# Optimization experiments

Hardware: AMD Instinct MI355X
Metric: run time of the kernel (lower is better)

## Reference

```python
import jax, jax.numpy as jnp
import numpy as np

B, T, D = 4, 2048, 1024
H, DK = 8, 64
EPS = 1e-6

def _xavier(key, shape):
    fan_in, fan_out = shape[1], shape[0]
    lim = float(np.sqrt(6.0 / (fan_in + fan_out)))
    return jax.random.uniform(key, shape, jnp.float32, -lim, lim)

def setup_inputs() -> dict:
    key = jax.random.key(0)
    ks = jax.random.split(key, 7)
    x = jax.random.normal(ks[0], (B, T, D), jnp.float32)
    W_Q = _xavier(ks[1], (H * DK, D))
    W_K = _xavier(ks[2], (H * DK, D))
    W_V = _xavier(ks[3], (H * DK, D))
    W_g_w = _xavier(ks[4], (H * DK, D))
    W_g_b = jax.random.normal(ks[5], (H * DK,), jnp.float32) * 0.02
    W_O = _xavier(ks[6], (D, H * DK))
    decay_log = jnp.zeros((H,), jnp.float32)
    return {"x": x, "W_Q": W_Q, "W_K": W_K, "W_V": W_V,
            "W_g_w": W_g_w, "W_g_b": W_g_b, "W_O": W_O,
            "decay_log": decay_log}

def _phi(u):
    # ELU + 1 feature map (positive)
    return jax.nn.elu(u) + 1.0

def reference(x, W_Q, W_K, W_V, W_g_w, W_g_b, W_O, decay_log):
    b, t, d = x.shape
    q = _phi((x @ W_Q.T).reshape(b, t, H, DK))
    k = _phi((x @ W_K.T).reshape(b, t, H, DK))
    v = (x @ W_V.T).reshape(b, t, H, DK)
    gamma = jax.nn.sigmoid(decay_log)           # [H]
    g4 = gamma[None, :, None, None]             # [1,H,1,1]
    g3 = gamma[None, :, None]                   # [1,H,1]

    # time-major for scan: [T,B,H,DK]
    qT = jnp.moveaxis(q, 1, 0)
    kT = jnp.moveaxis(k, 1, 0)
    vT = jnp.moveaxis(v, 1, 0)

    S0 = jnp.zeros((b, H, DK, DK), x.dtype)
    z0 = jnp.zeros((b, H, DK), x.dtype)

    def step(carry, inp):
        S, z = carry
        qt, kt, vt = inp
        S = g4 * S + jnp.einsum('bhi,bhj->bhij', kt, vt)
        z = g3 * z + kt
        num = jnp.einsum('bhij,bhi->bhj', S, qt)
        den = jnp.sum(z * qt, axis=-1, keepdims=True) + EPS
        return (S, z), num / den

    _, ys = jax.lax.scan(step, (S0, z0), (qT, kT, vT))  # ys: [T,B,H,DK]
    outputs = jnp.moveaxis(ys, 0, 1)                    # [B,T,H,DK]

    gate = jax.nn.sigmoid(x @ W_g_w.T + W_g_b).reshape(b, t, H, DK)
    y = (outputs * gate).reshape(b, t, H * DK)
    return y @ W_O.T
```

## Files before the change

kernel.cpp:

```cpp
#include <hip/hip_runtime.h>
#include <cstdint>
#include <cstddef>

#define B_   4
#define T_   2048
#define D_   1024
#define H_   8
#define DK_  64
#define HD_  512
#define CH_  64
#define NC_  32
#define EPS_ 1e-6f

typedef __attribute__((ext_vector_type(4))) float f32x4;
typedef __attribute__((ext_vector_type(8))) short s16x8;

__device__ __forceinline__ unsigned short f2bf(float f) {
    unsigned int x = __float_as_uint(f);
    unsigned int r = (x + 0x7FFFu + ((x >> 16) & 1u)) >> 16;
    return (unsigned short)r;
}
__device__ __forceinline__ float bf2f(unsigned short u) {
    return __uint_as_float(((unsigned int)u) << 16);
}
__device__ __forceinline__ void ld4(const float* p, float* o) {
    float4 v = *(const float4*)p; o[0]=v.x; o[1]=v.y; o[2]=v.z; o[3]=v.w;
}
__device__ __forceinline__ void gl_lds16(const unsigned short* g, unsigned short* l) {
    __builtin_amdgcn_global_load_lds(
        (const __attribute__((address_space(1))) unsigned int*)g,
        (__attribute__((address_space(3))) unsigned int*)l, 16, 0, 0);
}

__global__ __launch_bounds__(256) void k_cvt_all(
    const float* __restrict__ x,
    const float* __restrict__ wq, const float* __restrict__ wk,
    const float* __restrict__ wv, const float* __restrict__ wgw,
    const float* __restrict__ wo,
    unsigned short* __restrict__ xb,
    unsigned short* __restrict__ wqb, unsigned short* __restrict__ wkb,
    unsigned short* __restrict__ wvb, unsigned short* __restrict__ wgb,
    unsigned short* __restrict__ wob)
{
    int bid = blockIdx.x;
    const float* src; unsigned short* dst; int idx;
    if (bid < 8192) {
        src = x; dst = xb; idx = bid * 256 + threadIdx.x;
    } else {
        int r = bid - 8192;
        int w = r >> 9;
        idx = (r & 511) * 256 + threadIdx.x;
        switch (w) {
            case 0:  src = wq;  dst = wqb; break;
            case 1:  src = wk;  dst = wkb; break;
            case 2:  src = wv;  dst = wvb; break;
            case 3:  src = wgw; dst = wgb; break;
            default: src = wo;  dst = wob; break;
        }
    }
    float4 v = ((const float4*)src)[idx];
    ushort4 o;
    o.x = f2bf(v.x); o.y = f2bf(v.y); o.z = f2bf(v.z); o.w = f2bf(v.w);
    ((ushort4*)dst)[idx] = o;
}


__global__ __launch_bounds__(512, 2) void k_gemm_qkvg(
    const unsigned short* __restrict__ xb,
    const unsigned short* __restrict__ wqb, const unsigned short* __restrict__ wkb,
    const unsigned short* __restrict__ wvb, const unsigned short* __restrict__ wgb,
    const float* __restrict__ bias,
    unsigned short* __restrict__ qo, unsigned short* __restrict__ ko,
    unsigned short* __restrict__ vo, unsigned short* __restrict__ go)
{
    __shared__ unsigned short As[2][256 * 64];
    __shared__ unsigned short Bs[2][256 * 64];
    const int tid = threadIdx.x;
    const int id  = blockIdx.x;
    const int xcd = id & 7, per = id >> 3;
    const int mtile = xcd * 4 + (per & 3);
    const int ntile = per >> 2;
    const int which = ntile >> 1;
    const int nb    = ntile & 1;
    const int m0    = mtile * 256;
    const int n0    = nb * 256;
    const unsigned short* Wp = (which == 0) ? wqb : (which == 1) ? wkb : (which == 2) ? wvb : wgb;
    unsigned short* Op       = (which == 0) ? qo  : (which == 1) ? ko  : (which == 2) ? vo  : go;
    const int K = D_;
    const int NIT = K / 64;

    const int lane = tid & 63, wave = tid >> 6;
    const int wm = (wave >> 2) * 128, wn = (wave & 3) * 64;
    const int r16 = lane & 15, quad = lane >> 4;
    const int lrow = lane >> 3, lseg = lane & 7;
    const int sseg = lseg ^ lrow;
    const int rx   = r16 & 7;

    f32x4 acc[8][4];
    #pragma unroll
    for (int a = 0; a < 8; a++)
        #pragma unroll
        for (int b = 0; b < 4; b++) acc[a][b] = 0.0f;

    auto stage = [&](int buf, int ko_) {
        #pragma unroll
        for (int i = 0; i < 4; i++) {
            int chunk = wave * 4 + i;
            int row = chunk * 8 + lrow;
            gl_lds16(xb + (size_t)(m0 + row) * K + ko_ + sseg * 8, &As[buf][chunk * 512]);
            gl_lds16(Wp + (size_t)(n0 + row) * K + ko_ + sseg * 8, &Bs[buf][chunk * 512]);
        }
    };

    stage(0, 0);
    for (int it = 0; it < NIT; ++it) {
        if (it + 1 < NIT) {
            stage((it + 1) & 1, (it + 1) * 64);
            asm volatile("s_waitcnt vmcnt(8)" ::: "memory");
        } else {
            asm volatile("s_waitcnt vmcnt(0)" ::: "memory");
        }
        __builtin_amdgcn_s_barrier();
        const int buf = it & 1;
        #pragma unroll
        for (int kk = 0; kk < 64; kk += 32) {
            const int gb_ = kk >> 3;
            s16x8 af[8], bf[4];
            #pragma unroll
            for (int mt = 0; mt < 8; mt++)
                af[mt] = *(const s16x8*)&As[buf][(wm + mt * 16 + r16) * 64 + (((gb_ + quad) ^ rx) << 3)];
            #pragma unroll
            for (int nt = 0; nt < 4; nt++)
                bf[nt] = *(const s16x8*)&Bs[buf][(wn + nt * 16 + r16) * 64 + (((gb_ + quad) ^ rx) << 3)];
            #pragma unroll
            for (int mt = 0; mt < 8; mt++)
                #pragma unroll
                for (int nt = 0; nt < 4; nt++)
                    acc[mt][nt] = __builtin_amdgcn_mfma_f32_16x16x32_bf16(af[mt], bf[nt], acc[mt][nt], 0, 0, 0);
        }
        __builtin_amdgcn_s_barrier();
    }
    #pragma unroll
    for (int mt = 0; mt < 8; mt++) {
        #pragma unroll
        for (int nt = 0; nt < 4; nt++) {
            int col = n0 + wn + nt * 16 + r16;
            float bv = (which == 3) ? bias[col] : 0.0f;
            #pragma unroll
            for (int r = 0; r < 4; r++) {
                int row = m0 + wm + mt * 16 + quad * 4 + r;
                float v = acc[mt][nt][r];
                if (which <= 1)      v = (v > 0.0f) ? v + 1.0f : __builtin_expf(v);
                else if (which == 3) v = 1.0f / (1.0f + __builtin_expf(-(v + bv)));
                Op[(size_t)row * HD_ + col] = f2bf(v);
            }
        }
    }
}

__global__ __launch_bounds__(512, 2) void k_gemm_out(
    const unsigned short* __restrict__ ogb, const unsigned short* __restrict__ wob,
    float* __restrict__ y)
{
    __shared__ unsigned short As[2][256 * 64];
    __shared__ unsigned short Bs[2][128 * 64];
    const int tid = threadIdx.x;
    const int id  = blockIdx.x;
    const int xcd = id & 7, per = id >> 3;
    const int m0 = (xcd * 4 + (per & 3)) * 256;
    const int n0 = (per >> 2) * 128;
    const int K = HD_;
    const int NIT = K / 64;

    const int lane = tid & 63, wave = tid >> 6;
    const int wm = (wave >> 1) * 64, wn = (wave & 1) * 64;
    const int r16 = lane & 15, quad = lane >> 4;
    const int lrow = lane >> 3, lseg = lane & 7;
    const int sseg = lseg ^ lrow;
    const int rx   = r16 & 7;

    f32x4 acc[4][4];
    #pragma unroll
    for (int a = 0; a < 4; a++)
        #pragma unroll
        for (int b = 0; b < 4; b++) acc[a][b] = 0.0f;

    auto stage = [&](int buf, int ko_) {
        #pragma unroll
        for (int i = 0; i < 4; i++) {
            int chunk = wave * 4 + i;
            int row = chunk * 8 + lrow;
            gl_lds16(ogb + (size_t)(m0 + row) * K + ko_ + sseg * 8, &As[buf][chunk * 512]);
        }
        #pragma unroll
        for (int i = 0; i < 2; i++) {
            int chunk = wave * 2 + i;
            int row = chunk * 8 + lrow;
            gl_lds16(wob + (size_t)(n0 + row) * K + ko_ + sseg * 8, &Bs[buf][chunk * 512]);
        }
    };

    stage(0, 0);
    for (int it = 0; it < NIT; ++it) {
        if (it + 1 < NIT) {
            stage((it + 1) & 1, (it + 1) * 64);
            asm volatile("s_waitcnt vmcnt(6)" ::: "memory");
        } else {
            asm volatile("s_waitcnt vmcnt(0)" ::: "memory");
        }
        __builtin_amdgcn_s_barrier();
        const int buf = it & 1;
        #pragma unroll
        for (int kk = 0; kk < 64; kk += 32) {
            const int gb_ = kk >> 3;
            s16x8 af[4], bf[4];
            #pragma unroll
            for (int mt = 0; mt < 4; mt++)
                af[mt] = *(const s16x8*)&As[buf][(wm + mt * 16 + r16) * 64 + (((gb_ + quad) ^ rx) << 3)];
            #pragma unroll
            for (int nt = 0; nt < 4; nt++)
                bf[nt] = *(const s16x8*)&Bs[buf][(wn + nt * 16 + r16) * 64 + (((gb_ + quad) ^ rx) << 3)];
            #pragma unroll
            for (int mt = 0; mt < 4; mt++)
                #pragma unroll
                for (int nt = 0; nt < 4; nt++)
                    acc[mt][nt] = __builtin_amdgcn_mfma_f32_16x16x32_bf16(af[mt], bf[nt], acc[mt][nt], 0, 0, 0);
        }
        __builtin_amdgcn_s_barrier();
    }
    #pragma unroll
    for (int mt = 0; mt < 4; mt++)
        #pragma unroll
        for (int nt = 0; nt < 4; nt++) {
            int col = n0 + wn + nt * 16 + r16;
            #pragma unroll
            for (int r = 0; r < 4; r++) {
                int row = m0 + wm + mt * 16 + quad * 4 + r;
                y[(size_t)row * D_ + col] = acc[mt][nt][r];
            }
        }
}

__global__ __launch_bounds__(256) void k_chunk_sums(
    const unsigned short* __restrict__ Kb, const unsigned short* __restrict__ Vb,
    float* __restrict__ Ssum, float* __restrict__ zsum, const float* __restrict__ decay_log)
{
    __shared__ float kl[CH_ * 68];
    __shared__ float vl[CH_ * 68];
    const int tid = threadIdx.x;
    const int bc  = blockIdx.x;
    const int c   = bc & (NC_ - 1);
    const int bh  = bc >> 5;
    const int h   = bh & (H_ - 1);
    const int b   = bh >> 3;
    const float g  = 1.0f / (1.0f + __builtin_expf(-decay_log[h]));
    const float lg = __builtin_log2f(g);
    const int t0 = c * CH_;

    #pragma unroll
    for (int e = 0; e < 2; e++) {
        int lid = e * 256 + tid;
        int l = lid >> 3, d0 = (lid & 7) * 8;
        float w = __builtin_exp2f((float)(CH_ - 1 - l) * lg);
        size_t gidx = (size_t)(b * T_ + t0 + l) * HD_ + h * DK_ + d0;
        uint4 kraw = *(const uint4*)(Kb + gidx);
        uint4 vraw = *(const uint4*)(Vb + gidx);
        const unsigned short* kp = (const unsigned short*)&kraw;
        const unsigned short* vp = (const unsigned short*)&vraw;
        #pragma unroll
        for (int j = 0; j < 8; j++) {
            kl[l * 68 + d0 + j] = bf2f(kp[j]) * w;
            vl[l * 68 + d0 + j] = bf2f(vp[j]);
        }
    }
    __syncthreads();

    const int ti = tid >> 4, tj = tid & 15;
    const int i0 = ti * 4, j0 = tj * 4;
    float acc[4][4];
    #pragma unroll
    for (int r = 0; r < 4; r++)
        #pragma unroll
        for (int cc = 0; cc < 4; cc++) acc[r][cc] = 0.0f;

    for (int l = 0; l < CH_; l++) {
        float kv[4], vv[4];
        ld4(&kl[l * 68 + i0], kv);
        ld4(&vl[l * 68 + j0], vv);
        #pragma unroll
        for (int r = 0; r < 4; r++)
            #pragma unroll
            for (int cc = 0; cc < 4; cc++) acc[r][cc] += kv[r] * vv[cc];
    }
    size_t base = (size_t)bc * (DK_ * DK_);
    #pragma unroll
    for (int r = 0; r < 4; r++) {
        float4 st = make_float4(acc[r][0], acc[r][1], acc[r][2], acc[r][3]);
        *(float4*)&Ssum[base + (size_t)(i0 + r) * DK_ + j0] = st;
    }
    if (tid < DK_) {
        float s = 0.0f;
        for (int l = 0; l < CH_; l++) s += kl[l * 68 + tid];
        zsum[(size_t)bc * DK_ + tid] = s;
    }
}

__global__ __launch_bounds__(128) void k_chunk_scan(
    float* __restrict__ Ssum, float* __restrict__ zsum, const float* __restrict__ decay_log)
{
    const int tid = threadIdx.x;
    const int grp = blockIdx.x & 31;
    const int bh  = blockIdx.x >> 5;
    const int h   = bh & (H_ - 1);
    const float g  = 1.0f / (1.0f + __builtin_expf(-decay_log[h]));
    const float gC = __builtin_exp2f((float)CH_ * __builtin_log2f(g));
    int elem = grp * 128 + tid;
    float s = 0.0f;
    for (int c = 0; c < NC_; c++) {
        size_t idx = ((size_t)(bh * NC_ + c)) * 4096 + elem;
        float v = Ssum[idx];
        Ssum[idx] = s;
        s = gC * s + v;
    }
    if (grp == 0 && tid < DK_) {
        float z = 0.0f;
        for (int c = 0; c < NC_; c++) {
            size_t idx = ((size_t)(bh * NC_ + c)) * DK_ + tid;
            float v = zsum[idx];
            zsum[idx] = z;
            z = gC * z + v;
        }
    }
}

__global__ __launch_bounds__(256) void k_chunk_out(
    const unsigned short* __restrict__ Qb, const unsigned short* __restrict__ Kb,
    const unsigned short* __restrict__ Vb, const unsigned short* __restrict__ Gb,
    const float* __restrict__ Ssum, const float* __restrict__ zsum,
    unsigned short* __restrict__ OGb, const float* __restrict__ decay_log)
{
    __shared__ float BufA[CH_ * 68];
    __shared__ float BufB[CH_ * 68];
    __shared__ float BufC[CH_ * 68];
    __shared__ float den_l[CH_];
    __shared__ float zp_l[DK_];
    __shared__ float gpow[CH_ + 1];

    const int tid = threadIdx.x;
    const int bc  = blockIdx.x;
    const int c   = bc & (NC_ - 1);
    const int bh  = bc >> 5;
    const int h   = bh & (H_ - 1);
    const int b   = bh >> 3;
    const float g  = 1.0f / (1.0f + __builtin_expf(-decay_log[h]));
    const float lg = __builtin_log2f(g);
    const int t0 = c * CH_;

    if (tid <= CH_) gpow[tid] = __builtin_exp2f((float)tid * lg);
    if (tid < DK_)  zp_l[tid] = zsum[(size_t)bc * DK_ + tid];

    #pragma unroll
    for (int e = 0; e < 2; e++) {
        int lid = e * 256 + tid;
        int l = lid >> 3, d0 = (lid & 7) * 8;
        size_t gidx = (size_t)(b * T_ + t0 + l) * HD_ + h * DK_ + d0;
        uint4 qraw = *(const uint4*)(Qb + gidx);
        uint4 kraw = *(const uint4*)(Kb + gidx);
        const unsigned short* qp = (const unsigned short*)&qraw;
        const unsigned short* kp = (const unsigned short*)&kraw;
        #pragma unroll
        for (int j = 0; j < 8; j++) {
            BufA[(d0 + j) * 68 + l] = bf2f(qp[j]);
            BufB[(d0 + j) * 68 + l] = bf2f(kp[j]);
        }
    }
    {
        size_t base = (size_t)bc * 4096;
        #pragma unroll
        for (int e = 0; e < 4; e++) {
            int flat = (e * 256 + tid) * 4;
            int row = flat >> 6, c0 = flat & 63;
            *(float4*)&BufC[row * 68 + c0] = *(const float4*)&Ssum[base + flat];
        }
    }
    __syncthreads();

    const int ti = tid >> 4, tj = tid & 15;
    const int i0 = ti * 4, j0 = tj * 4;
    float sc[4][4], it[4][4];
    #pragma unroll
    for (int r = 0; r < 4; r++)
        #pragma unroll
        for (int cc = 0; cc < 4; cc++) { sc[r][cc] = 0.0f; it[r][cc] = 0.0f; }

    for (int d = 0; d < DK_; d++) {
        float qv[4], kv[4], sv[4];
        ld4(&BufA[d * 68 + i0], qv);
        ld4(&BufB[d * 68 + j0], kv);
        ld4(&BufC[d * 68 + j0], sv);
        #pragma unroll
        for (int r = 0; r < 4; r++)
            #pragma unroll
            for (int cc = 0; cc < 4; cc++) {
                sc[r][cc] += qv[r] * kv[cc];
                it[r][cc] += qv[r] * sv[cc];
            }
    }
    #pragma unroll
    for (int r = 0; r < 4; r++) {
        int i = i0 + r;
        #pragma unroll
        for (int cc = 0; cc < 4; cc++) {
            int jl = j0 + cc;
            sc[r][cc] = (jl <= i) ? sc[r][cc] * gpow[i - jl] : 0.0f;
            it[r][cc] *= gpow[i + 1];
        }
        float rs = sc[r][0] + sc[r][1] + sc[r][2] + sc[r][3];
        rs += __shfl_xor(rs, 1);
        rs += __shfl_xor(rs, 2);
        rs += __shfl_xor(rs, 4);
        rs += __shfl_xor(rs, 8);
        if (tj == 0) den_l[i] = rs;
    }
    __syncthreads();
    if (tid < DK_) {
        float dp = 0.0f;
        for (int d = 0; d < DK_; d++) dp += BufA[d * 68 + tid] * zp_l[d];
        den_l[tid] += gpow[tid + 1] * dp + EPS_;
    }
    __syncthreads();
    #pragma unroll
    for (int cc = 0; cc < 4; cc++) {
        float4 st = make_float4(sc[0][cc], sc[1][cc], sc[2][cc], sc[3][cc]);
        *(float4*)&BufA[(j0 + cc) * 68 + i0] = st;
    }
    #pragma unroll
    for (int e = 0; e < 2; e++) {
        int lid = e * 256 + tid;
        int l = lid >> 3, d0 = (lid & 7) * 8;
        size_t gidx = (size_t)(b * T_ + t0 + l) * HD_ + h * DK_ + d0;
        uint4 vraw = *(const uint4*)(Vb + gidx);
        const unsigned short* vp = (const unsigned short*)&vraw;
        #pragma unroll
        for (int j = 0; j < 8; j++) BufB[l * 68 + d0 + j] = bf2f(vp[j]);
    }
    __syncthreads();

    float og[4][4];
    #pragma unroll
    for (int r = 0; r < 4; r++)
        #pragma unroll
        for (int cc = 0; cc < 4; cc++) og[r][cc] = it[r][cc];

    for (int jl = 0; jl < CH_; jl++) {
        float scv[4], vv[4];
        ld4(&BufA[jl * 68 + i0], scv);
        ld4(&BufB[jl * 68 + j0], vv);
        #pragma unroll
        for (int r = 0; r < 4; r++)
            #pragma unroll
            for (int cc = 0; cc < 4; cc++) og[r][cc] += scv[r] * vv[cc];
    }
    #pragma unroll
    for (int r = 0; r < 4; r++) {
        int i = i0 + r;
        float rcp = 1.0f / den_l[i];
        size_t gidx = (size_t)(b * T_ + t0 + i) * HD_ + h * DK_ + j0;
        ushort4 graw = *(const ushort4*)(Gb + gidx);
        ushort4 o;
        o.x = f2bf(og[r][0] * rcp * bf2f(graw.x));
        o.y = f2bf(og[r][1] * rcp * bf2f(graw.y));
        o.z = f2bf(og[r][2] * rcp * bf2f(graw.z));
        o.w = f2bf(og[r][3] * rcp * bf2f(graw.w));
        *(ushort4*)(OGb + gidx) = o;
    }
}

extern "C" void kernel_launch(void* const* d_in, const int* in_sizes, int n_in,
                              void* d_out, int out_size, void* d_ws, size_t ws_size,
                              hipStream_t stream)
{
    (void)in_sizes; (void)n_in; (void)out_size; (void)ws_size;
    const float* x         = (const float*)d_in[0];
    const float* W_Q       = (const float*)d_in[1];
    const float* W_K       = (const float*)d_in[2];
    const float* W_V       = (const float*)d_in[3];
    const float* W_gw      = (const float*)d_in[4];
    const float* W_gb      = (const float*)d_in[5];
    const float* W_O       = (const float*)d_in[6];
    const float* decay_log = (const float*)d_in[7];
    float* y = (float*)d_out;

    char* ws = (char*)d_ws;
    size_t off = 0;
    auto alloc = [&](size_t bytes) { void* p = ws + off; off += (bytes + 255) & ~(size_t)255; return p; };
    unsigned short* xb   = (unsigned short*)alloc((size_t)B_ * T_ * D_ * 2);
    unsigned short* wqb  = (unsigned short*)alloc((size_t)HD_ * D_ * 2);
    unsigned short* wkb  = (unsigned short*)alloc((size_t)HD_ * D_ * 2);
    unsigned short* wvb  = (unsigned short*)alloc((size_t)HD_ * D_ * 2);
    unsigned short* wgb  = (unsigned short*)alloc((size_t)HD_ * D_ * 2);
    unsigned short* wob  = (unsigned short*)alloc((size_t)D_ * HD_ * 2);
    unsigned short* qb   = (unsigned short*)alloc((size_t)B_ * T_ * HD_ * 2);
    unsigned short* kb   = (unsigned short*)alloc((size_t)B_ * T_ * HD_ * 2);
    unsigned short* vb   = (unsigned short*)alloc((size_t)B_ * T_ * HD_ * 2);
    unsigned short* gb   = (unsigned short*)alloc((size_t)B_ * T_ * HD_ * 2);
    unsigned short* ogb  = (unsigned short*)alloc((size_t)B_ * T_ * HD_ * 2);
    float* Ssum = (float*)alloc((size_t)B_ * H_ * NC_ * DK_ * DK_ * 4);
    float* zsum = (float*)alloc((size_t)B_ * H_ * NC_ * DK_ * 4);

    k_cvt_all<<<8192 + 5 * 512, 256, 0, stream>>>(x, W_Q, W_K, W_V, W_gw, W_O,
                                                  xb, wqb, wkb, wvb, wgb, wob);
    k_gemm_qkvg<<<256, 512, 0, stream>>>(xb, wqb, wkb, wvb, wgb, W_gb, qb, kb, vb, gb);
    k_chunk_sums<<<B_ * H_ * NC_, 256, 0, stream>>>(kb, vb, Ssum, zsum, decay_log);
    k_chunk_scan<<<B_ * H_ * NC_, 128, 0, stream>>>(Ssum, zsum, decay_log);
    k_chunk_out<<<B_ * H_ * NC_, 256, 0, stream>>>(qb, kb, vb, gb, Ssum, zsum, ogb, decay_log);
    k_gemm_out<<<256, 512, 0, stream>>>(ogb, wob, y);
}
```

Baseline: 210.7 us.

## Interleave LDS reads, global prefetch and MFMA clusters in projection GEMMs

Both the QKVG projection GEMM and the output projection GEMM are restructured so each K-tile runs as several phases. Each phase reads fragments from LDS, issues a split A or B global-to-LDS prefetch for the next tile, then runs an MFMA cluster at raised wave priority behind sched_barrier fences. The aim is to overlap memory traffic with matrix-core work and cut fragment register pressure by loading half the A fragments at a time. The cost is many more workgroup barriers per iteration and a full vmcnt(0) wait at the top of each tile, which removes the earlier partial-wait prefetch overlap.

```diff
diff --git a/kernel.cpp b/kernel.cpp
--- a/kernel.cpp
+++ b/kernel.cpp
@@ -102,42 +102,96 @@
         #pragma unroll
         for (int b = 0; b < 4; b++) acc[a][b] = 0.0f;
 
-    auto stage = [&](int buf, int ko_) {
+    auto stageA = [&](int buf, int ko_) {
         #pragma unroll
         for (int i = 0; i < 4; i++) {
             int chunk = wave * 4 + i;
             int row = chunk * 8 + lrow;
             gl_lds16(xb + (size_t)(m0 + row) * K + ko_ + sseg * 8, &As[buf][chunk * 512]);
+        }
+    };
+    auto stageB = [&](int buf, int ko_) {
+        #pragma unroll
+        for (int i = 0; i < 4; i++) {
+            int chunk = wave * 4 + i;
+            int row = chunk * 8 + lrow;
             gl_lds16(Wp + (size_t)(n0 + row) * K + ko_ + sseg * 8, &Bs[buf][chunk * 512]);
         }
     };
-
-    stage(0, 0);
+    auto rdA = [&](int buf, int row, int gb) -> s16x8 {
+        return *(const s16x8*)&As[buf][row * 64 + (((gb + quad) ^ rx) << 3)];
+    };
+    auto rdB = [&](int buf, int row, int gb) -> s16x8 {
+        return *(const s16x8*)&Bs[buf][row * 64 + (((gb + quad) ^ rx) << 3)];
+    };
+
+    stageA(0, 0); stageB(0, 0);
     for (int it = 0; it < NIT; ++it) {
-        if (it + 1 < NIT) {
-            stage((it + 1) & 1, (it + 1) * 64);
-            asm volatile("s_waitcnt vmcnt(8)" ::: "memory");
-        } else {
-            asm volatile("s_waitcnt vmcnt(0)" ::: "memory");
-        }
-        __builtin_amdgcn_s_barrier();
         const int buf = it & 1;
-        #pragma unroll
-        for (int kk = 0; kk < 64; kk += 32) {
-            const int gb_ = kk >> 3;
-            s16x8 af[8], bf[4];
-            #pragma unroll
-            for (int mt = 0; mt < 8; mt++)
-                af[mt] = *(const s16x8*)&As[buf][(wm + mt * 16 + r16) * 64 + (((gb_ + quad) ^ rx) << 3)];
+        asm volatile("s_waitcnt vmcnt(0)" ::: "memory");
+        __builtin_amdgcn_s_barrier();
+
+        s16x8 af[4], bfr[4];
+        #pragma unroll
+        for (int mt = 0; mt < 4; mt++) af[mt]  = rdA(buf, wm + mt * 16 + r16, 0);
+        #pragma unroll
+        for (int nt = 0; nt < 4; nt++) bfr[nt] = rdB(buf, wn + nt * 16 + r16, 0);
+        if (it + 1 < NIT) stageA(buf ^ 1, (it + 1) * 64);
+        __builtin_amdgcn_s_barrier();
+        asm volatile("s_waitcnt lgkmcnt(0)" ::: "memory");
+        __builtin_amdgcn_sched_barrier(0);
+        __builtin_amdgcn_s_setprio(1);
+        #pragma unroll
+        for (int mt = 0; mt < 4; mt++)
             #pragma unroll
             for (int nt = 0; nt < 4; nt++)
-                bf[nt] = *(const s16x8*)&Bs[buf][(wn + nt * 16 + r16) * 64 + (((gb_ + quad) ^ rx) << 3)];
-            #pragma unroll
-            for (int mt = 0; mt < 8; mt++)
-                #pragma unroll
-                for (int nt = 0; nt < 4; nt++)
-                    acc[mt][nt] = __builtin_amdgcn_mfma_f32_16x16x32_bf16(af[mt], bf[nt], acc[mt][nt], 0, 0, 0);
-        }
+                acc[mt][nt] = __builtin_amdgcn_mfma_f32_16x16x32_bf16(af[mt], bfr[nt], acc[mt][nt], 0, 0, 0);
+        __builtin_amdgcn_s_setprio(0);
+        __builtin_amdgcn_s_barrier();
+
+        #pragma unroll
+        for (int mt = 0; mt < 4; mt++) af[mt] = rdA(buf, wm + (mt + 4) * 16 + r16, 0);
+        if (it + 1 < NIT) stageB(buf ^ 1, (it + 1) * 64);
+        __builtin_amdgcn_s_barrier();
+        asm volatile("s_waitcnt lgkmcnt(0)" ::: "memory");
+        __builtin_amdgcn_sched_barrier(0);
+        __builtin_amdgcn_s_setprio(1);
+        #pragma unroll
+        for (int mt = 0; mt < 4; mt++)
+            #pragma unroll
+            for (int nt = 0; nt < 4; nt++)
+                acc[mt + 4][nt] = __builtin_amdgcn_mfma_f32_16x16x32_bf16(af[mt], bfr[nt], acc[mt + 4][nt], 0, 0, 0);
+        __builtin_amdgcn_s_setprio(0);
+        __builtin_amdgcn_s_barrier();
+
+        #pragma unroll
+        for (int mt = 0; mt < 4; mt++) af[mt]  = rdA(buf, wm + mt * 16 + r16, 4);
+        #pragma unroll
+        for (int nt = 0; nt < 4; nt++) bfr[nt] = rdB(buf, wn + nt * 16 + r16, 4);
+        __builtin_amdgcn_s_barrier();
+        asm volatile("s_waitcnt lgkmcnt(0)" ::: "memory");
+        __builtin_amdgcn_sched_barrier(0);
+        __builtin_amdgcn_s_setprio(1);
+        #pragma unroll
+        for (int mt = 0; mt < 4; mt++)
+            #pragma unroll
+            for (int nt = 0; nt < 4; nt++)
+                acc[mt][nt] = __builtin_amdgcn_mfma_f32_16x16x32_bf16(af[mt], bfr[nt], acc[mt][nt], 0, 0, 0);
+        __builtin_amdgcn_s_setprio(0);
+        __builtin_amdgcn_s_barrier();
+
+        #pragma unroll
+        for (int mt = 0; mt < 4; mt++) af[mt] = rdA(buf, wm + (mt + 4) * 16 + r16, 4);
+        __builtin_amdgcn_s_barrier();
+        asm volatile("s_waitcnt lgkmcnt(0)" ::: "memory");
+        __builtin_amdgcn_sched_barrier(0);
+        __builtin_amdgcn_s_setprio(1);
+        #pragma unroll
+        for (int mt = 0; mt < 4; mt++)
+            #pragma unroll
+            for (int nt = 0; nt < 4; nt++)
+                acc[mt + 4][nt] = __builtin_amdgcn_mfma_f32_16x16x32_bf16(af[mt], bfr[nt], acc[mt + 4][nt], 0, 0, 0);
+        __builtin_amdgcn_s_setprio(0);
         __builtin_amdgcn_s_barrier();
     }
     #pragma unroll
@@ -185,13 +239,15 @@
         #pragma unroll
         for (int b = 0; b < 4; b++) acc[a][b] = 0.0f;
 
-    auto stage = [&](int buf, int ko_) {
+    auto stageA = [&](int buf, int ko_) {
         #pragma unroll
         for (int i = 0; i < 4; i++) {
             int chunk = wave * 4 + i;
             int row = chunk * 8 + lrow;
             gl_lds16(ogb + (size_t)(m0 + row) * K + ko_ + sseg * 8, &As[buf][chunk * 512]);
         }
+    };
+    auto stageB = [&](int buf, int ko_) {
         #pragma unroll
         for (int i = 0; i < 2; i++) {
             int chunk = wave * 2 + i;
@@ -199,33 +255,52 @@
             gl_lds16(wob + (size_t)(n0 + row) * K + ko_ + sseg * 8, &Bs[buf][chunk * 512]);
         }
     };
-
-    stage(0, 0);
+    auto rdA = [&](int buf, int row, int gb) -> s16x8 {
+        return *(const s16x8*)&As[buf][row * 64 + (((gb + quad) ^ rx) << 3)];
+    };
+    auto rdB = [&](int buf, int row, int gb) -> s16x8 {
+        return *(const s16x8*)&Bs[buf][row * 64 + (((gb + quad) ^ rx) << 3)];
+    };
+
+    stageA(0, 0); stageB(0, 0);
     for (int it = 0; it < NIT; ++it) {
-        if (it + 1 < NIT) {
-            stage((it + 1) & 1, (it + 1) * 64);
-            asm volatile("s_waitcnt vmcnt(6)" ::: "memory");
-        } else {
-            asm volatile("s_waitcnt vmcnt(0)" ::: "memory");
-        }
-        __builtin_amdgcn_s_barrier();
         const int buf = it & 1;
-        #pragma unroll
-        for (int kk = 0; kk < 64; kk += 32) {
-            const int gb_ = kk >> 3;
-            s16x8 af[4], bf[4];
-            #pragma unroll
-            for (int mt = 0; mt < 4; mt++)
-                af[mt] = *(const s16x8*)&As[buf][(wm + mt * 16 + r16) * 64 + (((gb_ + quad) ^ rx) << 3)];
+        asm volatile("s_waitcnt vmcnt(0)" ::: "memory");
+        __builtin_amdgcn_s_barrier();
+
+        s16x8 af[4], bfr[4];
+        #pragma unroll
+        for (int mt = 0; mt < 4; mt++) af[mt]  = rdA(buf, wm + mt * 16 + r16, 0);
+        #pragma unroll
+        for (int nt = 0; nt < 4; nt++) bfr[nt] = rdB(buf, wn + nt * 16 + r16, 0);
+        if (it + 1 < NIT) stageA(buf ^ 1, (it + 1) * 64);
+        __builtin_amdgcn_s_barrier();
+        asm volatile("s_waitcnt lgkmcnt(0)" ::: "memory");
+        __builtin_amdgcn_sched_barrier(0);
+        __builtin_amdgcn_s_setprio(1);
+        #pragma unroll
+        for (int mt = 0; mt < 4; mt++)
             #pragma unroll
             for (int nt = 0; nt < 4; nt++)
-                bf[nt] = *(const s16x8*)&Bs[buf][(wn + nt * 16 + r16) * 64 + (((gb_ + quad) ^ rx) << 3)];
-            #pragma unroll
-            for (int mt = 0; mt < 4; mt++)
-                #pragma unroll
-                for (int nt = 0; nt < 4; nt++)
-                    acc[mt][nt] = __builtin_amdgcn_mfma_f32_16x16x32_bf16(af[mt], bf[nt], acc[mt][nt], 0, 0, 0);
-        }
+                acc[mt][nt] = __builtin_amdgcn_mfma_f32_16x16x32_bf16(af[mt], bfr[nt], acc[mt][nt], 0, 0, 0);
+        __builtin_amdgcn_s_setprio(0);
+        __builtin_amdgcn_s_barrier();
+
+        #pragma unroll
+        for (int mt = 0; mt < 4; mt++) af[mt]  = rdA(buf, wm + mt * 16 + r16, 4);
+        #pragma unroll
+        for (int nt = 0; nt < 4; nt++) bfr[nt] = rdB(buf, wn + nt * 16 + r16, 4);
+        if (it + 1 < NIT) stageB(buf ^ 1, (it + 1) * 64);
+        __builtin_amdgcn_s_barrier();
+        asm volatile("s_waitcnt lgkmcnt(0)" ::: "memory");
+        __builtin_amdgcn_sched_barrier(0);
+        __builtin_amdgcn_s_setprio(1);
+        #pragma unroll
+        for (int mt = 0; mt < 4; mt++)
+            #pragma unroll
+            for (int nt = 0; nt < 4; nt++)
+                acc[mt][nt] = __builtin_amdgcn_mfma_f32_16x16x32_bf16(af[mt], bfr[nt], acc[mt][nt], 0, 0, 0);
+        __builtin_amdgcn_s_setprio(0);
         __builtin_amdgcn_s_barrier();
     }
     #pragma unroll
```

New measurement: 214.8 us. About the same (+2.0%).

## Use bf16 MFMA for intra-chunk scores and inter-chunk state in chunk_out

Applied to the files above, without the earlier changes.

Replaces the scalar FP32 outer-product loops for Q·K^T scores and Q·S inter-chunk terms in the chunk output kernel with bf16 16x16x32 MFMA instructions. Q and K stay in bf16 in LDS, and the state S is stored transposed (via the chunk-state kernel writing S^T) and converted to bf16. V is loaded up front alongside Q and K. This cuts ALU work in the attention-like stage at the cost of rounding the state and scores to bf16 and using more LDS.

```diff
diff --git a/kernel.cpp b/kernel.cpp
--- a/kernel.cpp
+++ b/kernel.cpp
@@ -63,7 +63,6 @@
     o.x = f2bf(v.x); o.y = f2bf(v.y); o.z = f2bf(v.z); o.w = f2bf(v.w);
     ((ushort4*)dst)[idx] = o;
 }
-
 
 __global__ __launch_bounds__(512, 2) void k_gemm_qkvg(
     const unsigned short* __restrict__ xb,
@@ -275,7 +274,7 @@
     }
     __syncthreads();
 
-    const int ti = tid >> 4, tj = tid & 15;
+    const int ti = tid & 15, tj = tid >> 4;
     const int i0 = ti * 4, j0 = tj * 4;
     float acc[4][4];
     #pragma unroll
@@ -294,9 +293,9 @@
     }
     size_t base = (size_t)bc * (DK_ * DK_);
     #pragma unroll
-    for (int r = 0; r < 4; r++) {
-        float4 st = make_float4(acc[r][0], acc[r][1], acc[r][2], acc[r][3]);
-        *(float4*)&Ssum[base + (size_t)(i0 + r) * DK_ + j0] = st;
+    for (int cc = 0; cc < 4; cc++) {
+        float4 st = make_float4(acc[0][cc], acc[1][cc], acc[2][cc], acc[3][cc]);
+        *(float4*)&Ssum[base + (size_t)(j0 + cc) * DK_ + i0] = st;
     }
     if (tid < DK_) {
         float s = 0.0f;
@@ -339,11 +338,14 @@
     const float* __restrict__ Ssum, const float* __restrict__ zsum,
     unsigned short* __restrict__ OGb, const float* __restrict__ decay_log)
 {
-    __shared__ float BufA[CH_ * 68];
-    __shared__ float BufB[CH_ * 68];
-    __shared__ float BufC[CH_ * 68];
-    __shared__ float den_l[CH_];
-    __shared__ float zp_l[DK_];
+    __shared__ unsigned short ql[64 * 72];
+    __shared__ unsigned short kl[64 * 72];
+    __shared__ unsigned short sT[64 * 72];
+    __shared__ float scT[64 * 68];
+    __shared__ float vf [64 * 68];
+    __shared__ float ogl[64 * 68];
+    __shared__ float den_l[64];
+    __shared__ float zp[64];
     __shared__ float gpow[CH_ + 1];
 
     const int tid = threadIdx.x;
@@ -357,7 +359,7 @@
     const int t0 = c * CH_;
 
     if (tid <= CH_) gpow[tid] = __builtin_exp2f((float)tid * lg);
-    if (tid < DK_)  zp_l[tid] = zsum[(size_t)bc * DK_ + tid];
+    if (tid < DK_)  zp[tid] = zsum[(size_t)bc * DK_ + tid];
 
     #pragma unroll
     for (int e = 0; e < 2; e++) {
@@ -366,96 +368,103 @@
         size_t gidx = (size_t)(b * T_ + t0 + l) * HD_ + h * DK_ + d0;
         uint4 qraw = *(const uint4*)(Qb + gidx);
         uint4 kraw = *(const uint4*)(Kb + gidx);
-        const unsigned short* qp = (const unsigned short*)&qraw;
-        const unsigned short* kp = (const unsigned short*)&kraw;
-        #pragma unroll
-        for (int j = 0; j < 8; j++) {
-            BufA[(d0 + j) * 68 + l] = bf2f(qp[j]);
-            BufB[(d0 + j) * 68 + l] = bf2f(kp[j]);
-        }
+        uint4 vraw = *(const uint4*)(Vb + gidx);
+        *(uint4*)&ql[l * 72 + d0] = qraw;
+        *(uint4*)&kl[l * 72 + d0] = kraw;
+        const unsigned short* vp = (const unsigned short*)&vraw;
+        #pragma unroll
+        for (int j = 0; j < 8; j++) vf[l * 68 + d0 + j] = bf2f(vp[j]);
     }
     {
-        size_t base = (size_t)bc * 4096;
+        int j = tid >> 2, seg = tid & 3;
+        const float4* src = (const float4*)&Ssum[(size_t)bc * 4096 + (size_t)j * 64 + seg * 16];
         #pragma unroll
         for (int e = 0; e < 4; e++) {
-            int flat = (e * 256 + tid) * 4;
-            int row = flat >> 6, c0 = flat & 63;
-            *(float4*)&BufC[row * 68 + c0] = *(const float4*)&Ssum[base + flat];
-        }
+            float4 a4 = src[e];
+            ushort4 o;
+            o.x = f2bf(a4.x); o.y = f2bf(a4.y); o.z = f2bf(a4.z); o.w = f2bf(a4.w);
+            *(ushort4*)&sT[j * 72 + seg * 16 + e * 4] = o;
+        }
+    }
+    __syncthreads();
+
+    const int lane = tid & 63, wave = tid >> 6;
+    const int r16 = lane & 15, quad = lane >> 4;
+    const int ibase = 16 * wave;
+
+    f32x4 sc4[4];
+    #pragma unroll
+    for (int lt = 0; lt < 4; lt++) {
+        f32x4 s = 0.0f;
+        #pragma unroll
+        for (int ks = 0; ks < 2; ks++) {
+            s16x8 af  = *(const s16x8*)&ql[(ibase + r16) * 72 + ks * 32 + quad * 8];
+            s16x8 bf_ = *(const s16x8*)&kl[(16 * lt + r16) * 72 + ks * 32 + quad * 8];
+            s = __builtin_amdgcn_mfma_f32_16x16x32_bf16(af, bf_, s, 0, 0, 0);
+        }
+        sc4[lt] = s;
+    }
+    float rs[4] = {0.0f, 0.0f, 0.0f, 0.0f};
+    #pragma unroll
+    for (int lt = 0; lt < 4; lt++) {
+        int l = 16 * lt + r16;
+        #pragma unroll
+        for (int rr = 0; rr < 4; rr++) {
+            int i = ibase + quad * 4 + rr;
+            float val = (l <= i) ? sc4[lt][rr] * gpow[i - l] : 0.0f;
+            scT[l * 68 + i] = val;
+            rs[rr] += val;
+        }
+    }
+    #pragma unroll
+    for (int rr = 0; rr < 4; rr++) {
+        float v_ = rs[rr];
+        v_ += __shfl_xor(v_, 1);
+        v_ += __shfl_xor(v_, 2);
+        v_ += __shfl_xor(v_, 4);
+        v_ += __shfl_xor(v_, 8);
+        if (r16 == 0) den_l[ibase + quad * 4 + rr] = v_;
+    }
+    #pragma unroll
+    for (int jt = 0; jt < 4; jt++) {
+        f32x4 o = 0.0f;
+        #pragma unroll
+        for (int ks = 0; ks < 2; ks++) {
+            s16x8 af  = *(const s16x8*)&ql[(ibase + r16) * 72 + ks * 32 + quad * 8];
+            s16x8 bf_ = *(const s16x8*)&sT[(16 * jt + r16) * 72 + ks * 32 + quad * 8];
+            o = __builtin_amdgcn_mfma_f32_16x16x32_bf16(af, bf_, o, 0, 0, 0);
+        }
+        #pragma unroll
+        for (int rr = 0; rr < 4; rr++) {
+            int i = ibase + quad * 4 + rr;
+            ogl[i * 68 + 16 * jt + r16] = o[rr] * gpow[i + 1];
+        }
+    }
+    __syncthreads();
+
+    if (tid < DK_) {
+        float dp = 0.0f;
+        #pragma unroll
+        for (int d8 = 0; d8 < 8; d8++) {
+            uint4 qq = *(const uint4*)&ql[tid * 72 + d8 * 8];
+            const unsigned short* qp = (const unsigned short*)&qq;
+            #pragma unroll
+            for (int e = 0; e < 8; e++) dp += bf2f(qp[e]) * zp[d8 * 8 + e];
+        }
+        den_l[tid] += gpow[tid + 1] * dp + EPS_;
     }
     __syncthreads();
 
     const int ti = tid >> 4, tj = tid & 15;
     const int i0 = ti * 4, j0 = tj * 4;
-    float sc[4][4], it[4][4];
-    #pragma unroll
-    for (int r = 0; r < 4; r++)
-        #pragma unroll
-        for (int cc = 0; cc < 4; cc++) { sc[r][cc] = 0.0f; it[r][cc] = 0.0f; }
-
-    for (int d = 0; d < DK_; d++) {
-        float qv[4], kv[4], sv[4];
-        ld4(&BufA[d * 68 + i0], qv);
-        ld4(&BufB[d * 68 + j0], kv);
-        ld4(&BufC[d * 68 + j0], sv);
-        #pragma unroll
-        for (int r = 0; r < 4; r++)
-            #pragma unroll
-            for (int cc = 0; cc < 4; cc++) {
-                sc[r][cc] += qv[r] * kv[cc];
-                it[r][cc] += qv[r] * sv[cc];
-            }
-    }
-    #pragma unroll
-    for (int r = 0; r < 4; r++) {
-        int i = i0 + r;
-        #pragma unroll
-        for (int cc = 0; cc < 4; cc++) {
-            int jl = j0 + cc;
-            sc[r][cc] = (jl <= i) ? sc[r][cc] * gpow[i - jl] : 0.0f;
-            it[r][cc] *= gpow[i + 1];
-        }
-        float rs = sc[r][0] + sc[r][1] + sc[r][2] + sc[r][3];
-        rs += __shfl_xor(rs, 1);
-        rs += __shfl_xor(rs, 2);
-        rs += __shfl_xor(rs, 4);
-        rs += __shfl_xor(rs, 8);
-        if (tj == 0) den_l[i] = rs;
-    }
-    __syncthreads();
-    if (tid < DK_) {
-        float dp = 0.0f;
-        for (int d = 0; d < DK_; d++) dp += BufA[d * 68 + tid] * zp_l[d];
-        den_l[tid] += gpow[tid + 1] * dp + EPS_;
-    }
-    __syncthreads();
-    #pragma unroll
-    for (int cc = 0; cc < 4; cc++) {
-        float4 st = make_float4(sc[0][cc], sc[1][cc], sc[2][cc], sc[3][cc]);
-        *(float4*)&BufA[(j0 + cc) * 68 + i0] = st;
-    }
-    #pragma unroll
-    for (int e = 0; e < 2; e++) {
-        int lid = e * 256 + tid;
-        int l = lid >> 3, d0 = (lid & 7) * 8;
-        size_t gidx = (size_t)(b * T_ + t0 + l) * HD_ + h * DK_ + d0;
-        uint4 vraw = *(const uint4*)(Vb + gidx);
-        const unsigned short* vp = (const unsigned short*)&vraw;
-        #pragma unroll
-        for (int j = 0; j < 8; j++) BufB[l * 68 + d0 + j] = bf2f(vp[j]);
-    }
-    __syncthreads();
-
     float og[4][4];
     #pragma unroll
-    for (int r = 0; r < 4; r++)
-        #pragma unroll
-        for (int cc = 0; cc < 4; cc++) og[r][cc] = it[r][cc];
-
-    for (int jl = 0; jl < CH_; jl++) {
+    for (int r = 0; r < 4; r++) ld4(&ogl[(i0 + r) * 68 + j0], og[r]);
+
+    for (int l = 0; l < CH_; l++) {
         float scv[4], vv[4];
-        ld4(&BufA[jl * 68 + i0], scv);
-        ld4(&BufB[jl * 68 + j0], vv);
+        ld4(&scT[l * 68 + i0], scv);
+        ld4(&vf[l * 68 + j0], vv);
         #pragma unroll
         for (int r = 0; r < 4; r++)
             #pragma unroll
```

New measurement: 205.4 us. 1.03x faster.
